# Kernel optimization log

Measured on AMD Instinct MI355X. Metric: run time of the kernel, lower is better.

## Reference

```python
import jax, jax.numpy as jnp
import numpy as np

NEG_SLOPE = 0.2  # PyG GATConv default leaky_relu slope
EPS = 1e-16


def gat_layer(x, src, dst, n, W, a_src, a_dst, b, heads, ch):
    # x: [N, F_in] -> h: [N, H, C]
    h = (x @ W).reshape(n, heads, ch)
    # per-node attention logits (cheaper than per-edge dot products)
    e_src = jnp.einsum('nhc,hc->nh', h, a_src)  # [N, H]
    e_dst = jnp.einsum('nhc,hc->nh', h, a_dst)  # [N, H]
    e = jax.nn.leaky_relu(e_src[src] + e_dst[dst], NEG_SLOPE)  # [E, H]
    # segment softmax over incoming edges of each target node
    m = jax.ops.segment_max(e, dst, num_segments=n)            # [N, H]
    ex = jnp.exp(e - m[dst])
    denom = jax.ops.segment_sum(ex, dst, num_segments=n)       # [N, H]
    alpha = ex / (denom[dst] + EPS)                            # [E, H]
    # attention-weighted scatter-add of source features
    out = jax.ops.segment_sum(h[src] * alpha[:, :, None], dst, num_segments=n)  # [N, H, C]
    # concat=False -> mean over heads, then bias
    return out.mean(axis=1) + b


def reference(x, edge_index, W0, as0, ad0, b0, W1, as1, ad1, b1, W2, as2, ad2, b2):
    n = x.shape[0]
    # PyG GATConv add_self_loops=True
    loops = jnp.arange(n, dtype=edge_index.dtype)
    src = jnp.concatenate([edge_index[0], loops])
    dst = jnp.concatenate([edge_index[1], loops])
    heads = as0.shape[0]
    x = gat_layer(x, src, dst, n, W0, as0, ad0, b0, heads, as0.shape[1])
    x = gat_layer(x, src, dst, n, W1, as1, ad1, b1, heads, as1.shape[1])
    x = gat_layer(x, src, dst, n, W2, as2, ad2, b2, heads, as2.shape[1])
    return x


def setup_inputs() -> dict:
    key = jax.random.key(0)
    N, E = 10000, 160000
    F_IN, HID, OUT, H = 512, 256, 256, 4
    ks = jax.random.split(key, 16)
    inp = {}
    inp['x'] = jax.random.normal(ks[0], (N, F_IN), dtype=jnp.float32)
    inp['edge_index'] = jax.random.randint(ks[1], (2, E), 0, N, dtype=jnp.int32)
    dims = [(F_IN, HID), (HID, HID), (HID, OUT)]
    for i, (fi, fo) in enumerate(dims):
        scale = 1.0 / np.sqrt(fi)
        inp[f'W{i}'] = jax.random.normal(ks[2 + 4 * i], (fi, H * fo), dtype=jnp.float32) * scale
        inp[f'as{i}'] = jax.random.normal(ks[3 + 4 * i], (H, fo), dtype=jnp.float32) * 0.1
        inp[f'ad{i}'] = jax.random.normal(ks[4 + 4 * i], (H, fo), dtype=jnp.float32) * 0.1
        inp[f'b{i}'] = jnp.zeros((fo,), dtype=jnp.float32)
    return inp
```

## Files before the change

### kernel.cpp

```cpp
#include <hip/hip_runtime.h>
#include <hip/hip_fp16.h>
#include <math.h>

#define HEADS 4
#define CH 256
#define HC 1024
#define NSLICE 4
#define NEG_SLOPE 0.2f
#define MAXS 320
#define ASCALE (1.0f / 1024.0f)

typedef _Float16 f16x8 __attribute__((ext_vector_type(8)));
typedef _Float16 f16x4 __attribute__((ext_vector_type(4)));
typedef __attribute__((ext_vector_type(4))) float f32x4;

static inline int cdiv(int a, int b) { return (a + b - 1) / b; }

__device__ __forceinline__ __half2 u2h2(unsigned u) {
  union {
    unsigned u;
    __half2 h;
  } x;
  x.u = u;
  return x.h;
}
__device__ __forceinline__ unsigned h22u(__half2 h) {
  union {
    __half2 h;
    unsigned u;
  } x;
  x.h = h;
  return x.u;
}
__device__ __forceinline__ void gload_lds16(const void* g, void* l) {
  __builtin_amdgcn_global_load_lds((const __attribute__((address_space(1))) void*)g,
                                   (__attribute__((address_space(3))) void*)l, 16, 0, 0);
}

__global__ void k_count(const int* __restrict__ ei, int E, int ET, int* __restrict__ cnt) {
  int e = blockIdx.x * blockDim.x + threadIdx.x;
  if (e >= ET) return;
  int d = (e < E) ? ei[E + e] : (e - E);
  atomicAdd(&cnt[d], 1);
}

__global__ __launch_bounds__(1024) void k_scan(const int* __restrict__ counts,
                                               int* __restrict__ offsets, int n) {
  __shared__ int wsum[16];
  __shared__ int carry_s;
  int lane = threadIdx.x & 63, wv = threadIdx.x >> 6;
  if (threadIdx.x == 0) carry_s = 0;
  __syncthreads();
  for (int base = 0; base < n; base += 1024) {
    int i = base + threadIdx.x;
    int orig = (i < n) ? counts[i] : 0;
    int v = orig;
#pragma unroll
    for (int off = 1; off < 64; off <<= 1) {
      int t = __shfl_up(v, off);
      if (lane >= off) v += t;
    }
    if (lane == 63) wsum[wv] = v;
    __syncthreads();
    int carry = carry_s;
    int wpre = 0;
#pragma unroll
    for (int w = 0; w < 16; w++) wpre += (w < wv) ? wsum[w] : 0;
    int incl = v + wpre;
    if (i < n) offsets[i] = carry + incl - orig;
    __syncthreads();
    if (threadIdx.x == 1023) carry_s = carry + incl;
    __syncthreads();
  }
  if (threadIdx.x == 0) offsets[n] = carry_s;
}

__global__ void k_fill(const int* __restrict__ ei, int E, int ET,
                       const int* __restrict__ offsets, int* __restrict__ cursor,
                       int2* __restrict__ esd) {
  int e = blockIdx.x * blockDim.x + threadIdx.x;
  if (e >= ET) return;
  int s = (e < E) ? ei[e] : (e - E);
  int d = (e < E) ? ei[E + e] : (e - E);
  int pos = offsets[d] + atomicAdd(&cursor[d], 1);
  esd[pos] = make_int2(s, d);
}

__global__ __launch_bounds__(256) void k_transpose_w(const float* __restrict__ W,
                                                     _Float16* __restrict__ Wt, int K) {
  __shared__ float tile[32][33];
  int tx = threadIdx.x & 31, ty = threadIdx.x >> 5;
  int k0 = blockIdx.x * 32, n0 = blockIdx.y * 32;
#pragma unroll
  for (int r = ty; r < 32; r += 8) tile[r][tx] = W[(size_t)(k0 + r) * HC + n0 + tx];
  __syncthreads();
#pragma unroll
  for (int r = ty; r < 32; r += 8)
    Wt[(size_t)(n0 + r) * K + k0 + tx] = (_Float16)tile[tx][r];
}

__global__ void k_cast_f16(const float* __restrict__ in, _Float16* __restrict__ out, int n) {
  int i = (blockIdx.x * blockDim.x + threadIdx.x) * 8;
  if (i >= n) return;
  float4 a = *(const float4*)&in[i];
  float4 b = *(const float4*)&in[i + 4];
  f16x8 o;
  o[0] = (_Float16)a.x;
  o[1] = (_Float16)a.y;
  o[2] = (_Float16)a.z;
  o[3] = (_Float16)a.w;
  o[4] = (_Float16)b.x;
  o[5] = (_Float16)b.y;
  o[6] = (_Float16)b.z;
  o[7] = (_Float16)b.w;
  *(f16x8*)&out[i] = o;
}

__global__ __launch_bounds__(256) void k_gemm_mfma(const _Float16* __restrict__ A,
                                                   const _Float16* __restrict__ Bt,
                                                   _Float16* __restrict__ hsl, int M, int K) {
  __shared__ _Float16 sA[2][128 * 32];
  __shared__ _Float16 sB[2][128 * 32];
  int t = threadIdx.x;
  int lane = t & 63, wv = t >> 6;
  int wr = wv >> 1, wc = wv & 1;
  int row0 = blockIdx.x * 128, col0 = blockIdx.y * 128;
  int l15 = lane & 15, l4 = lane >> 4;

  f32x4 acc[4][4] = {};

  auto stage = [&](_Float16* sdst, const _Float16* g, int grow0, int rowmax, int k0) {
#pragma unroll
    for (int q = 0; q < 2; ++q) {
      int r = grow0 + q * 64 + (t >> 2);
      if (r > rowmax) r = rowmax;
      const _Float16* gp = g + (size_t)r * K + k0 + (t & 3) * 8;
      gload_lds16(gp, sdst + q * 2048 + t * 8);
    }
  };

  int KT = K / 32;
  stage(sA[0], A, row0, M - 1, 0);
  stage(sB[0], Bt, col0, HC - 1, 0);
  int cur = 0;
  for (int kt = 0; kt < KT; ++kt) {
    __syncthreads();
    if (kt + 1 < KT) {
      stage(sA[cur ^ 1], A, row0, M - 1, (kt + 1) * 32);
      stage(sB[cur ^ 1], Bt, col0, HC - 1, (kt + 1) * 32);
    }
    f16x8 af[4], bfr[4];
#pragma unroll
    for (int i = 0; i < 4; i++)
      af[i] = *(f16x8*)&sA[cur][(wr * 64 + i * 16 + l15) * 32 + l4 * 8];
#pragma unroll
    for (int j = 0; j < 4; j++)
      bfr[j] = *(f16x8*)&sB[cur][(wc * 64 + j * 16 + l15) * 32 + l4 * 8];
#pragma unroll
    for (int i = 0; i < 4; i++)
#pragma unroll
      for (int j = 0; j < 4; j++)
        acc[i][j] = __builtin_amdgcn_mfma_f32_16x16x32_f16(af[i], bfr[j], acc[i][j], 0, 0, 0);
    cur ^= 1;
  }
#pragma unroll
  for (int i = 0; i < 4; i++) {
#pragma unroll
    for (int j = 0; j < 4; j++) {
      int col = col0 + wc * 64 + j * 16 + l15;
      int head = col >> 8;
      int c = (col >> 6) & 3;
      int jj = col & 63;
      size_t sbase = ((size_t)c * M) * 256 + head * 64 + jj;
#pragma unroll
      for (int r = 0; r < 4; r++) {
        int row = row0 + wr * 64 + i * 16 + l4 * 4 + r;
        if (row < M) hsl[sbase + (size_t)row * 256] = (_Float16)acc[i][j][r];
      }
    }
  }
}

__global__ __launch_bounds__(256) void k_logits(const _Float16* __restrict__ hsl,
                                                const float* __restrict__ as_,
                                                const float* __restrict__ ad_,
                                                float* __restrict__ es, float* __restrict__ ed,
                                                int M) {
  __shared__ float lds_s[4][64];
  __shared__ float lds_d[4][64];
  int n = blockIdx.x;
  int t = threadIdx.x;
  int c = t >> 6, u = t & 63;
  f16x4 hv = *(const f16x4*)&hsl[((size_t)c * M + n) * 256 + u * 4];
  int head = u >> 4;
  int ch = head * 256 + c * 64 + (u & 15) * 4;
  float4 s4 = *(const float4*)&as_[ch];
  float4 d4 = *(const float4*)&ad_[ch];
  float h0 = (float)hv[0], h1 = (float)hv[1], h2 = (float)hv[2], h3 = (float)hv[3];
  float ds = h0 * s4.x + h1 * s4.y + h2 * s4.z + h3 * s4.w;
  float dd = h0 * d4.x + h1 * d4.y + h2 * d4.z + h3 * d4.w;
  lds_s[head][c * 16 + (u & 15)] = ds;
  lds_d[head][c * 16 + (u & 15)] = dd;
  __syncthreads();
  int wv = t >> 6, l = t & 63;
  float vs = lds_s[wv][l];
  float vd = lds_d[wv][l];
#pragma unroll
  for (int off = 32; off; off >>= 1) {
    vs += __shfl_xor(vs, off);
    vd += __shfl_xor(vd, off);
  }
  if (l == 0) {
    es[n * HEADS + wv] = vs;
    ed[n * HEADS + wv] = vd;
  }
}

__global__ __launch_bounds__(256) void k_aggregate(const _Float16* __restrict__ hsl,
                                                   const float4* __restrict__ es4,
                                                   const float4* __restrict__ ed4,
                                                   const float* __restrict__ es,
                                                   const float* __restrict__ ed,
                                                   const int* __restrict__ offsets,
                                                   const int2* __restrict__ esd,
                                                   const float* __restrict__ bias,
                                                   float* __restrict__ xout,
                                                   _Float16* __restrict__ xout_h, int N) {
  __shared__ uint4 s_ap[MAXS];
  __shared__ int s_src[MAXS];
  int c = blockIdx.x & 3;
  int nb = (blockIdx.x >> 2) * 4;
  int base = offsets[nb];
  int nend = (nb + 4 < N) ? nb + 4 : N;
  int total = offsets[nend] - base;
  int cap = total < MAXS ? total : MAXS;
  for (int idx = threadIdx.x; idx < cap; idx += 256) {
    int2 sd = esd[base + idx];
    float4 a = es4[sd.x], b = ed4[sd.y];
    float v0 = a.x + b.x, v1 = a.y + b.y, v2 = a.z + b.z, v3 = a.w + b.w;
    v0 = v0 > 0.f ? v0 : NEG_SLOPE * v0;
    v1 = v1 > 0.f ? v1 : NEG_SLOPE * v1;
    v2 = v2 > 0.f ? v2 : NEG_SLOPE * v2;
    v3 = v3 > 0.f ? v3 : NEG_SLOPE * v3;
    uint4 ap;
    ap.x = h22u(__float2half2_rn(__expf(v0) * ASCALE));
    ap.y = h22u(__float2half2_rn(__expf(v1) * ASCALE));
    ap.z = h22u(__float2half2_rn(__expf(v2) * ASCALE));
    ap.w = h22u(__float2half2_rn(__expf(v3) * ASCALE));
    s_ap[idx] = ap;
    s_src[idx] = sd.x;
  }
  __syncthreads();
  int n = nb + (threadIdx.x >> 6);
  if (n >= N) return;
  int lane = threadIdx.x & 63;
  int g = lane >> 5;
  int q = lane & 31;
  int hq = q >> 3;
  const _Float16* sl = hsl + (size_t)c * N * 256;
  const __half2* aph = (const __half2*)s_ap;
  __half2 z2 = __float2half2_rn(0.f);
  __half2 acc2[4] = {z2, z2, z2, z2};
  __half2 sum2 = z2;
  int k0 = offsets[n], k1 = offsets[n + 1];
  int r = k0 - base + g;
  int rend = k1 - base;
  if (total <= MAXS) {
    for (; r + 2 < rend; r += 4) {
      int sA = s_src[r], sB = s_src[r + 2];
      __half2 aA = aph[r * 4 + hq];
      __half2 aB = aph[(r + 2) * 4 + hq];
      uint4 hA = *(const uint4*)&sl[(size_t)sA * 256 + q * 8];
      uint4 hB = *(const uint4*)&sl[(size_t)sB * 256 + q * 8];
      sum2 = __hadd2(sum2, __hadd2(aA, aB));
      acc2[0] = __hfma2(aA, u2h2(hA.x), acc2[0]);
      acc2[1] = __hfma2(aA, u2h2(hA.y), acc2[1]);
      acc2[2] = __hfma2(aA, u2h2(hA.z), acc2[2]);
      acc2[3] = __hfma2(aA, u2h2(hA.w), acc2[3]);
      acc2[0] = __hfma2(aB, u2h2(hB.x), acc2[0]);
      acc2[1] = __hfma2(aB, u2h2(hB.y), acc2[1]);
      acc2[2] = __hfma2(aB, u2h2(hB.z), acc2[2]);
      acc2[3] = __hfma2(aB, u2h2(hB.w), acc2[3]);
    }
    if (r < rend) {
      int sA = s_src[r];
      __half2 aA = aph[r * 4 + hq];
      uint4 hA = *(const uint4*)&sl[(size_t)sA * 256 + q * 8];
      sum2 = __hadd2(sum2, aA);
      acc2[0] = __hfma2(aA, u2h2(hA.x), acc2[0]);
      acc2[1] = __hfma2(aA, u2h2(hA.y), acc2[1]);
      acc2[2] = __hfma2(aA, u2h2(hA.z), acc2[2]);
      acc2[3] = __hfma2(aA, u2h2(hA.w), acc2[3]);
    }
  } else {
    for (; r < rend; r += 2) {
      int2 sd = esd[base + r];
      float v = es[sd.x * 4 + hq] + ed[sd.y * 4 + hq];
      v = v > 0.f ? v : NEG_SLOPE * v;
      __half2 aA = __float2half2_rn(__expf(v) * ASCALE);
      uint4 hA = *(const uint4*)&sl[(size_t)sd.x * 256 + q * 8];
      sum2 = __hadd2(sum2, aA);
      acc2[0] = __hfma2(aA, u2h2(hA.x), acc2[0]);
      acc2[1] = __hfma2(aA, u2h2(hA.y), acc2[1]);
      acc2[2] = __hfma2(aA, u2h2(hA.z), acc2[2]);
      acc2[3] = __hfma2(aA, u2h2(hA.w), acc2[3]);
    }
  }
  float sa = __low2float(sum2);
  sa += __shfl_xor(sa, 32);
  float ia = 0.25f / (sa + 1e-20f);
  float acc[8];
#pragma unroll
  for (int j = 0; j < 4; j++) {
    acc[2 * j] = __low2float(acc2[j]) * ia;
    acc[2 * j + 1] = __high2float(acc2[j]) * ia;
  }
#pragma unroll
  for (int j = 0; j < 8; j++) {
    float v = acc[j];
    v += __shfl_xor(v, 8);
    v += __shfl_xor(v, 16);
    v += __shfl_xor(v, 32);
    acc[j] = v;
  }
  if (lane < 8) {
    int oc = c * 64 + lane * 8;
    if (xout) {
      float4 o0 = make_float4(acc[0] + bias[oc + 0], acc[1] + bias[oc + 1],
                              acc[2] + bias[oc + 2], acc[3] + bias[oc + 3]);
      float4 o1 = make_float4(acc[4] + bias[oc + 4], acc[5] + bias[oc + 5],
                              acc[6] + bias[oc + 6], acc[7] + bias[oc + 7]);
      *(float4*)&xout[(size_t)n * CH + oc] = o0;
      *(float4*)&xout[(size_t)n * CH + oc + 4] = o1;
    }
    if (xout_h) {
      f16x8 o;
#pragma unroll
      for (int j = 0; j < 8; j++) o[j] = (_Float16)(acc[j] + bias[oc + j]);
      *(f16x8*)&xout_h[(size_t)n * CH + oc] = o;
    }
  }
}

extern "C" void kernel_launch(void* const* d_in, const int* in_sizes, int n_in,
                              void* d_out, int out_size, void* d_ws, size_t ws_size,
                              hipStream_t stream) {
  const float* x = (const float*)d_in[0];
  const int* ei = (const int*)d_in[1];
  const float* W[3] = {(const float*)d_in[2], (const float*)d_in[6], (const float*)d_in[10]};
  const float* AS[3] = {(const float*)d_in[3], (const float*)d_in[7], (const float*)d_in[11]};
  const float* AD[3] = {(const float*)d_in[4], (const float*)d_in[8], (const float*)d_in[12]};
  const float* BI[3] = {(const float*)d_in[5], (const float*)d_in[9], (const float*)d_in[13]};
  const int N = in_sizes[0] / 512;
  const int E = in_sizes[1] / 2;
  const int ET = E + N;
  const int Kd[3] = {512, 256, 256};

  char* p = (char*)d_ws;
  auto alloc = [&](size_t bytes) {
    char* r = p;
    p += (bytes + 255) & ~(size_t)255;
    return (void*)r;
  };
  _Float16* hsl = (_Float16*)alloc((size_t)NSLICE * N * 256 * 2);
  _Float16* axh = (_Float16*)alloc((size_t)N * 512 * 2);
  _Float16* acth = (_Float16*)alloc((size_t)N * CH * 2);
  _Float16* Wt[3];
  for (int i = 0; i < 3; i++) Wt[i] = (_Float16*)alloc((size_t)HC * Kd[i] * 2);
  float* es = (float*)alloc((size_t)N * HEADS * 4);
  float* ed = (float*)alloc((size_t)N * HEADS * 4);
  int* offsets = (int*)alloc((size_t)(N + 1) * 4);
  int* cursor = (int*)alloc((size_t)N * 4);
  int2* esd = (int2*)alloc((size_t)ET * 8);

  hipMemsetAsync(cursor, 0, (size_t)N * 4, stream);
  k_count<<<cdiv(ET, 256), 256, 0, stream>>>(ei, E, ET, cursor);
  k_scan<<<1, 1024, 0, stream>>>(cursor, offsets, N);
  hipMemsetAsync(cursor, 0, (size_t)N * 4, stream);
  k_fill<<<cdiv(ET, 256), 256, 0, stream>>>(ei, E, ET, offsets, cursor, esd);

  for (int i = 0; i < 3; i++)
    k_transpose_w<<<dim3(Kd[i] / 32, HC / 32), 256, 0, stream>>>(W[i], Wt[i], Kd[i]);
  k_cast_f16<<<cdiv(N * 512, 8 * 256), 256, 0, stream>>>(x, axh, N * 512);

  const _Float16* ain = axh;
  int aggGrid = cdiv(N, 4) * NSLICE;
  for (int layer = 0; layer < 3; ++layer) {
    int K = Kd[layer];
    k_gemm_mfma<<<dim3(cdiv(N, 128), HC / 128), 256, 0, stream>>>(ain, Wt[layer], hsl, N, K);
    k_logits<<<N, 256, 0, stream>>>(hsl, AS[layer], AD[layer], es, ed, N);
    if (layer < 2) {
      k_aggregate<<<aggGrid, 256, 0, stream>>>(hsl, (const float4*)es, (const float4*)ed, es,
                                               ed, offsets, esd, BI[layer], (float*)nullptr,
                                               acth, N);
    } else {
      k_aggregate<<<aggGrid, 256, 0, stream>>>(hsl, (const float4*)es, (const float4*)ed, es,
                                               ed, offsets, esd, BI[layer], (float*)d_out,
                                               (_Float16*)nullptr, N);
    }
    ain = acth;
  }
}
```

Measured before the change: 228.2 us.

## Fuse attention logit computation into GEMM epilogue with atomic accumulation

```diff
diff --git a/kernel.cpp b/kernel.cpp
--- a/kernel.cpp
+++ b/kernel.cpp
@@ -118,7 +118,11 @@
 
 __global__ __launch_bounds__(256) void k_gemm_mfma(const _Float16* __restrict__ A,
                                                    const _Float16* __restrict__ Bt,
-                                                   _Float16* __restrict__ hsl, int M, int K) {
+                                                   _Float16* __restrict__ hsl,
+                                                   const float* __restrict__ as_,
+                                                   const float* __restrict__ ad_,
+                                                   float* __restrict__ es,
+                                                   float* __restrict__ ed, int M, int K) {
   __shared__ _Float16 sA[2][128 * 32];
   __shared__ _Float16 sB[2][128 * 32];
   int t = threadIdx.x;
@@ -179,40 +183,35 @@
       }
     }
   }
-}
-
-__global__ __launch_bounds__(256) void k_logits(const _Float16* __restrict__ hsl,
-                                                const float* __restrict__ as_,
-                                                const float* __restrict__ ad_,
-                                                float* __restrict__ es, float* __restrict__ ed,
-                                                int M) {
-  __shared__ float lds_s[4][64];
-  __shared__ float lds_d[4][64];
-  int n = blockIdx.x;
-  int t = threadIdx.x;
-  int c = t >> 6, u = t & 63;
-  f16x4 hv = *(const f16x4*)&hsl[((size_t)c * M + n) * 256 + u * 4];
-  int head = u >> 4;
-  int ch = head * 256 + c * 64 + (u & 15) * 4;
-  float4 s4 = *(const float4*)&as_[ch];
-  float4 d4 = *(const float4*)&ad_[ch];
-  float h0 = (float)hv[0], h1 = (float)hv[1], h2 = (float)hv[2], h3 = (float)hv[3];
-  float ds = h0 * s4.x + h1 * s4.y + h2 * s4.z + h3 * s4.w;
-  float dd = h0 * d4.x + h1 * d4.y + h2 * d4.z + h3 * d4.w;
-  lds_s[head][c * 16 + (u & 15)] = ds;
-  lds_d[head][c * 16 + (u & 15)] = dd;
-  __syncthreads();
-  int wv = t >> 6, l = t & 63;
-  float vs = lds_s[wv][l];
-  float vd = lds_d[wv][l];
-#pragma unroll
-  for (int off = 32; off; off >>= 1) {
-    vs += __shfl_xor(vs, off);
-    vd += __shfl_xor(vd, off);
-  }
-  if (l == 0) {
-    es[n * HEADS + wv] = vs;
-    ed[n * HEADS + wv] = vd;
+  {
+    int head = col0 >> 8;
+    int cb = head * 256 + (col0 & 255) + wc * 64 + l15;
+    float asv[4], adv[4];
+#pragma unroll
+    for (int j = 0; j < 4; j++) {
+      asv[j] = as_[cb + j * 16];
+      adv[j] = ad_[cb + j * 16];
+    }
+#pragma unroll
+    for (int i = 0; i < 4; i++) {
+#pragma unroll
+      for (int r = 0; r < 4; r++) {
+        float dsp = acc[i][0][r] * asv[0] + acc[i][1][r] * asv[1] + acc[i][2][r] * asv[2] +
+                    acc[i][3][r] * asv[3];
+        float ddp = acc[i][0][r] * adv[0] + acc[i][1][r] * adv[1] + acc[i][2][r] * adv[2] +
+                    acc[i][3][r] * adv[3];
+#pragma unroll
+        for (int off = 1; off < 16; off <<= 1) {
+          dsp += __shfl_xor(dsp, off);
+          ddp += __shfl_xor(ddp, off);
+        }
+        int row = row0 + wr * 64 + i * 16 + l4 * 4 + r;
+        if (l15 == 0 && row < M) {
+          atomicAdd(&es[row * 4 + head], dsp);
+          atomicAdd(&ed[row * 4 + head], ddp);
+        }
+      }
+    }
   }
 }
 
@@ -387,8 +386,9 @@
   int aggGrid = cdiv(N, 4) * NSLICE;
   for (int layer = 0; layer < 3; ++layer) {
     int K = Kd[layer];
-    k_gemm_mfma<<<dim3(cdiv(N, 128), HC / 128), 256, 0, stream>>>(ain, Wt[layer], hsl, N, K);
-    k_logits<<<N, 256, 0, stream>>>(hsl, AS[layer], AD[layer], es, ed, N);
+    hipMemsetAsync(es, 0, (size_t)N * HEADS * 4 * 2, stream);
+    k_gemm_mfma<<<dim3(cdiv(N, 128), HC / 128), 256, 0, stream>>>(
+        ain, Wt[layer], hsl, AS[layer], AD[layer], es, ed, N, K);
     if (layer < 2) {
       k_aggregate<<<aggGrid, 256, 0, stream>>>(hsl, (const float4*)es, (const float4*)ed, es,
                                                ed, offsets, esd, BI[layer], (float*)nullptr,
```

New measurement: 257.6 us. 1.13x slower.
